# Optimization experiments

Measured on AMD Instinct MI355X. Metric: run time of the kernel, lower is better.

Reference implementation:

```python
import jax, jax.numpy as jnp
import numpy as np

EMBED_DIM = 256
NUM_HEADS = 8
QKV_DIM = EMBED_DIM  # qkv_dim_ratio = 1
HEAD_DIM = QKV_DIM // NUM_HEADS  # 32


def setup_inputs() -> dict:
    key = jax.random.key(0)
    ks = jax.random.split(key, 6)
    B, C, H, W = 1, EMBED_DIM, 64, 64
    s = 0.02
    return {
        "x": jax.random.normal(ks[0], (B, C, H, W), dtype=jnp.float32),
        "wq": jax.random.normal(ks[1], (QKV_DIM, C), dtype=jnp.float32) * s,
        "wk": jax.random.normal(ks[2], (QKV_DIM, C), dtype=jnp.float32) * s,
        "wv": jax.random.normal(ks[3], (QKV_DIM, C), dtype=jnp.float32) * s,
        "wo": jax.random.normal(ks[4], (C, QKV_DIM), dtype=jnp.float32) * s,
        "wl": jax.random.normal(ks[5], (C, 1, 3, 3), dtype=jnp.float32) * s,
    }


def _mhsa(x, wq, wk, wv, wo, wl):
    B, C, H, W = x.shape
    N = H * W
    xf = x.reshape(B, C, N)  # 1x1 conv == channel matmul
    def proj(w):
        # [B, qkv, N] -> [B, heads, N, head_dim]
        y = jnp.einsum('oc,bcn->bon', w, xf)
        return y.reshape(B, NUM_HEADS, HEAD_DIM, N).transpose(0, 1, 3, 2)
    q, k, v = proj(wq), proj(wk), proj(wv)
    scale = HEAD_DIM ** -0.5
    attn = jax.nn.softmax(jnp.einsum('bhnd,bhmd->bhnm', q, k) * scale, axis=-1)
    out = jnp.einsum('bhnm,bhmd->bhnd', attn, v)  # [B, h, N, d]
    out = out.transpose(0, 1, 3, 2).reshape(B, QKV_DIM, N)
    attn_out = jnp.einsum('co,bon->bcn', wo, out).reshape(B, C, H, W)
    local_out = jax.lax.conv_general_dilated(
        x, wl, window_strides=(1, 1), padding=((1, 1), (1, 1)),
        dimension_numbers=('NCHW', 'OIHW', 'NCHW'), feature_group_count=C)
    return local_out + attn_out


def reference(x, wq, wk, wv, wo, wl):
    return _mhsa(x, wq, wk, wv, wo, wl)
```

## Files before the change

### kernel.cpp

```cpp
#include <hip/hip_runtime.h>

#define N_TOK 4096
#define C_DIM 256
#define HEADS 8
#define HDIM  32
#define KSPLIT 4
#define QSCALE 0.17677669529663687f
#define L2E    1.4426950408889634f

typedef __attribute__((ext_vector_type(8))) short bf16x8;
typedef __attribute__((ext_vector_type(4))) float f32x4;
typedef __attribute__((ext_vector_type(4))) unsigned int u32x4;
typedef __attribute__((ext_vector_type(8))) unsigned short u16x8;

static __device__ __forceinline__ unsigned short f2bf(float f) {
  union { float f; unsigned int u; } c; c.f = f;
  return (unsigned short)((c.u + 0x8000u) >> 16);
}
static __device__ __forceinline__ float bf2f(unsigned short u) {
  union { unsigned int i; float f; } c; c.i = ((unsigned int)u) << 16;
  return c.f;
}
static __device__ __forceinline__ float fexp2(float x) {
  float r; asm("v_exp_f32 %0, %1" : "=v"(r) : "v"(x)); return r;
}
static __device__ __forceinline__ unsigned int cvt_pk(float lo, float hi) {
  unsigned int r; asm("v_cvt_pk_bf16_f32 %0, %1, %2" : "=v"(r) : "v"(lo), "v"(hi)); return r;
}

__global__ __launch_bounds__(256) void wsplit(
    const float* __restrict__ wq, const float* __restrict__ wk,
    const float* __restrict__ wv, const float* __restrict__ wo,
    unsigned short* __restrict__ Whi, unsigned short* __restrict__ Wlo)
{
  const int i4  = blockIdx.x * 256 + threadIdx.x;
  const int idx = i4 * 4;
  const int r   = idx >> 8;
  const float* src; int off; float scl = 1.f;
  if (r < 256)      { src = wq; off = idx;          scl = QSCALE * L2E; }
  else if (r < 512) { src = wk; off = idx - 65536;  }
  else if (r < 768) { src = wv; off = idx - 131072; }
  else              { src = wo; off = idx - 196608; }
  float4 v = *reinterpret_cast<const float4*>(&src[off]);
  v.x *= scl; v.y *= scl; v.z *= scl; v.w *= scl;
  ushort4 h, l;
  h.x = f2bf(v.x); l.x = f2bf(v.x - bf2f(h.x));
  h.y = f2bf(v.y); l.y = f2bf(v.y - bf2f(h.y));
  h.z = f2bf(v.z); l.z = f2bf(v.z - bf2f(h.z));
  h.w = f2bf(v.w); l.w = f2bf(v.w - bf2f(h.w));
  *reinterpret_cast<ushort4*>(&Whi[idx]) = h;
  *reinterpret_cast<ushort4*>(&Wlo[idx]) = l;
}

__global__ __launch_bounds__(256) void tsplit(
    const float* __restrict__ src,
    unsigned short* __restrict__ dhi, unsigned short* __restrict__ dlo)
{
  __shared__ float T[64][69];
  const int c0 = blockIdx.y * 64, n0 = blockIdx.x * 64;
  const int t = threadIdx.x;
  {
    const int cl = t >> 2, ng = (t & 3) * 16;
    #pragma unroll
    for (int jj = 0; jj < 4; jj++) {
      const float4 v = *reinterpret_cast<const float4*>(&src[(c0 + cl) * N_TOK + n0 + ng + jj * 4]);
      T[cl][ng + jj * 4 + 0] = v.x; T[cl][ng + jj * 4 + 1] = v.y;
      T[cl][ng + jj * 4 + 2] = v.z; T[cl][ng + jj * 4 + 3] = v.w;
    }
  }
  __syncthreads();
  {
    const int nl = t >> 2, cg = (t & 3) * 16;
    u16x8 h0, h1, l0, l1;
    #pragma unroll
    for (int j = 0; j < 8; j++) {
      const float v = T[cg + j][nl];
      h0[j] = f2bf(v); l0[j] = f2bf(v - bf2f(h0[j]));
    }
    #pragma unroll
    for (int j = 0; j < 8; j++) {
      const float v = T[cg + 8 + j][nl];
      h1[j] = f2bf(v); l1[j] = f2bf(v - bf2f(h1[j]));
    }
    const size_t base = (size_t)(n0 + nl) * C_DIM + c0 + cg;
    *reinterpret_cast<u16x8*>(&dhi[base])     = h0;
    *reinterpret_cast<u16x8*>(&dhi[base + 8]) = h1;
    *reinterpret_cast<u16x8*>(&dlo[base])     = l0;
    *reinterpret_cast<u16x8*>(&dlo[base + 8]) = l1;
  }
}

__global__ __launch_bounds__(256) void qkv_mfma(
    const unsigned short* __restrict__ Whi, const unsigned short* __restrict__ Wlo,
    const unsigned short* __restrict__ Xhi, const unsigned short* __restrict__ Xlo,
    unsigned short* __restrict__ Qkv, unsigned short* __restrict__ Kt)
{
  const int n0 = blockIdx.x * 64;
  const int by = blockIdx.y;
  const int tid = threadIdx.x;
  const int w = tid >> 6, lane = tid & 63, lq = lane & 15, g = lane >> 4;
  const int o0 = by * 64 + w * 16;

  __shared__ unsigned short Bs[2][4096];

  const int e0l = tid & 63, e0f = tid >> 6;
  const unsigned short* s0p; const unsigned short* s1p;
  {
    const int lq_ = e0l & 15, g_ = e0l >> 4;
    const int f0 = e0f, f1 = e0f + 4;
    s0p = ((f0 & 1) ? Xlo : Xhi) + (size_t)(n0 + (f0 >> 1) * 16 + lq_) * C_DIM + 8 * g_;
    s1p = ((f1 & 1) ? Xlo : Xhi) + (size_t)(n0 + (f1 >> 1) * 16 + lq_) * C_DIM + 8 * g_;
  }
  const unsigned short* ahp = &Whi[(size_t)(o0 + lq) * C_DIM + 8 * g];
  const unsigned short* alp = &Wlo[(size_t)(o0 + lq) * C_DIM + 8 * g];

  f32x4 acc[4] = {{0.f,0.f,0.f,0.f},{0.f,0.f,0.f,0.f},{0.f,0.f,0.f,0.f},{0.f,0.f,0.f,0.f}};

  bf16x8 ah = *reinterpret_cast<const bf16x8*>(ahp);
  bf16x8 al = *reinterpret_cast<const bf16x8*>(alp);
  {
    const bf16x8 b0 = *reinterpret_cast<const bf16x8*>(s0p);
    const bf16x8 b1 = *reinterpret_cast<const bf16x8*>(s1p);
    *reinterpret_cast<bf16x8*>(&Bs[0][(size_t)tid * 8]) = b0;
    *reinterpret_cast<bf16x8*>(&Bs[0][((size_t)tid + 256) * 8]) = b1;
  }
  __syncthreads();

  int cur = 0;
  #pragma unroll
  for (int kk = 0; kk < 8; kk++) {
    bf16x8 nb0 = {}, nb1 = {}, nah = {}, nal = {};
    if (kk < 7) {
      const int ko = (kk + 1) * 32;
      nb0 = *reinterpret_cast<const bf16x8*>(s0p + ko);
      nb1 = *reinterpret_cast<const bf16x8*>(s1p + ko);
      nah = *reinterpret_cast<const bf16x8*>(ahp + ko);
      nal = *reinterpret_cast<const bf16x8*>(alp + ko);
    }
    #pragma unroll
    for (int ns = 0; ns < 4; ns++) {
      const bf16x8 bh = *reinterpret_cast<const bf16x8*>(&Bs[cur][(size_t)((ns * 2 + 0) * 64 + lane) * 8]);
      const bf16x8 bl = *reinterpret_cast<const bf16x8*>(&Bs[cur][(size_t)((ns * 2 + 1) * 64 + lane) * 8]);
      acc[ns] = __builtin_amdgcn_mfma_f32_16x16x32_bf16(ah, bh, acc[ns], 0, 0, 0);
      acc[ns] = __builtin_amdgcn_mfma_f32_16x16x32_bf16(ah, bl, acc[ns], 0, 0, 0);
      acc[ns] = __builtin_amdgcn_mfma_f32_16x16x32_bf16(al, bh, acc[ns], 0, 0, 0);
    }
    if (kk < 7) {
      *reinterpret_cast<bf16x8*>(&Bs[cur ^ 1][(size_t)tid * 8]) = nb0;
      *reinterpret_cast<bf16x8*>(&Bs[cur ^ 1][((size_t)tid + 256) * 8]) = nb1;
      ah = nah; al = nal;
    }
    __syncthreads();
    cur ^= 1;
  }

  if (by < 4 || by >= 8) {
    const int orow0 = (by < 4 ? by * 64 : (by - 8) * 64 + 512) + w * 16 + 4 * g;
    #pragma unroll
    for (int ns = 0; ns < 4; ns++)
      #pragma unroll
      for (int r = 0; r < 4; r++)
        Qkv[(size_t)(orow0 + r) * N_TOK + n0 + ns * 16 + lq] = f2bf(acc[ns][r]);
  } else {
    const int ok0 = (by - 4) * 64 + w * 16 + 4 * g;
    const int hh = ok0 >> 5, d0 = ok0 & 31;
    #pragma unroll
    for (int ns = 0; ns < 4; ns++) {
      ushort4 u;
      u.x = f2bf(acc[ns][0]); u.y = f2bf(acc[ns][1]);
      u.z = f2bf(acc[ns][2]); u.w = f2bf(acc[ns][3]);
      *reinterpret_cast<ushort4*>(&Kt[((size_t)hh * N_TOK + n0 + ns * 16 + lq) * HDIM + d0]) = u;
    }
  }
}

__global__ __launch_bounds__(256) void dwconv_kernel(
    const float* __restrict__ x, const float* __restrict__ wl,
    float* __restrict__ out)
{
  const int idx = blockIdx.x * 256 + threadIdx.x;
  const int c  = idx >> 12;
  const int yy = (idx >> 6) & 63;
  const int xx = idx & 63;
  const float* xc = x + c * 4096;
  const float* wc = wl + c * 9;
  float acc = 0.f;
  #pragma unroll
  for (int dy = 0; dy < 3; dy++) {
    const int y = yy + dy - 1;
    if (y < 0 || y > 63) continue;
    #pragma unroll
    for (int dx = 0; dx < 3; dx++) {
      const int x2 = xx + dx - 1;
      if (x2 < 0 || x2 > 63) continue;
      acc += wc[dy * 3 + dx] * xc[y * 64 + x2];
    }
  }
  out[idx] = acc;
}

__global__ __launch_bounds__(256) void attn_mfma(
    const unsigned short* __restrict__ Qkv,
    const unsigned short* __restrict__ Kt,
    float* __restrict__ Opart,
    float* __restrict__ lpart)
{
  const int h  = blockIdx.z;
  const int ks = blockIdx.y;
  const int tid  = threadIdx.x;
  const int w    = tid >> 6;
  const int lane = tid & 63;
  const int lq   = lane & 15;
  const int g    = lane >> 4;
  const int nqa  = blockIdx.x * 128 + w * 32 + lq;
  const int nqb  = nqa + 16;

  __shared__ unsigned short KbL[2][2048];
  __shared__ unsigned short VbL[2][2048];

  bf16x8 qfa, qfb;
  {
    const unsigned short* Qh = Qkv + h * HDIM * N_TOK;
    #pragma unroll
    for (int j = 0; j < 8; j++) {
      qfa[j] = (short)Qh[(8 * g + j) * N_TOK + nqa];
      qfb[j] = (short)Qh[(8 * g + j) * N_TOK + nqb];
    }
  }

  const unsigned short* KtH = Kt + (size_t)h * N_TOK * HDIM;
  const unsigned short* VH  = Qkv + (512 + h * HDIM) * N_TOK;
  const int kbase = ks * (N_TOK / KSPLIT);
  const int pr = 8 * (lq >> 2) + (lq & 3);

  const int skey  = (w & 1) * 4 + (w >> 1) * 32 + pr;
  const unsigned short* ksrc = &KtH[(size_t)(kbase + skey) * HDIM + 8 * g];
  const int sdrow = (w & 1) * 16 + lq;
  const unsigned short* vsrc = &VH[(size_t)sdrow * N_TOK + kbase + (w >> 1) * 32 + 8 * g];

  {
    const bf16x8 kr = *reinterpret_cast<const bf16x8*>(ksrc);
    const bf16x8 vr = *reinterpret_cast<const bf16x8*>(vsrc);
    *reinterpret_cast<bf16x8*>(&KbL[0][tid * 8]) = kr;
    *reinterpret_cast<bf16x8*>(&VbL[0][tid * 8]) = vr;
  }
  __syncthreads();

  f32x4 o0a = {0.f,0.f,0.f,0.f}, o1a = {0.f,0.f,0.f,0.f};
  f32x4 o0b = {0.f,0.f,0.f,0.f}, o1b = {0.f,0.f,0.f,0.f};
  f32x4 laa = {0.f,0.f,0.f,0.f}, lab = {0.f,0.f,0.f,0.f};
  const f32x4 zz = {0.f,0.f,0.f,0.f};
  constexpr int NT = (N_TOK / KSPLIT) / 64;

  int cur = 0;
  #pragma unroll 2
  for (int t = 0; t < NT; ++t) {
    bf16x8 kr = {}, vr = {};
    if (t + 1 < NT) {
      kr = *reinterpret_cast<const bf16x8*>(ksrc + (size_t)(t + 1) * 64 * HDIM);
      vr = *reinterpret_cast<const bf16x8*>(vsrc + (t + 1) * 64);
    }

    const unsigned short* kb = &KbL[cur][0];
    const unsigned short* vb = &VbL[cur][0];
    const bf16x8 kf0 = *reinterpret_cast<const bf16x8*>(&kb[lane * 8]);
    const bf16x8 kf1 = *reinterpret_cast<const bf16x8*>(&kb[lane * 8 + 512]);
    const bf16x8 kf2 = *reinterpret_cast<const bf16x8*>(&kb[lane * 8 + 1024]);
    const bf16x8 kf3 = *reinterpret_cast<const bf16x8*>(&kb[lane * 8 + 1536]);

    f32x4 s0 = __builtin_amdgcn_mfma_f32_16x16x32_bf16(kf0, qfa, zz, 0, 0, 0);
    f32x4 s1 = __builtin_amdgcn_mfma_f32_16x16x32_bf16(kf1, qfa, zz, 0, 0, 0);
    f32x4 s2 = __builtin_amdgcn_mfma_f32_16x16x32_bf16(kf2, qfa, zz, 0, 0, 0);
    f32x4 s3 = __builtin_amdgcn_mfma_f32_16x16x32_bf16(kf3, qfa, zz, 0, 0, 0);
    #pragma unroll
    for (int r = 0; r < 4; r++) {
      s0[r] = fexp2(s0[r]); s1[r] = fexp2(s1[r]);
      s2[r] = fexp2(s2[r]); s3[r] = fexp2(s3[r]);
    }
    laa += s0; laa += s1; laa += s2; laa += s3;
    const u32x4 pua_a = { cvt_pk(s0[0], s0[1]), cvt_pk(s0[2], s0[3]),
                          cvt_pk(s1[0], s1[1]), cvt_pk(s1[2], s1[3]) };
    const u32x4 pub_a = { cvt_pk(s2[0], s2[1]), cvt_pk(s2[2], s2[3]),
                          cvt_pk(s3[0], s3[1]), cvt_pk(s3[2], s3[3]) };
    const bf16x8 pfa_a = __builtin_bit_cast(bf16x8, pua_a);
    const bf16x8 pfb_a = __builtin_bit_cast(bf16x8, pub_a);

    f32x4 t0 = __builtin_amdgcn_mfma_f32_16x16x32_bf16(kf0, qfb, zz, 0, 0, 0);
    f32x4 t1 = __builtin_amdgcn_mfma_f32_16x16x32_bf16(kf1, qfb, zz, 0, 0, 0);
    f32x4 t2 = __builtin_amdgcn_mfma_f32_16x16x32_bf16(kf2, qfb, zz, 0, 0, 0);
    f32x4 t3 = __builtin_amdgcn_mfma_f32_16x16x32_bf16(kf3, qfb, zz, 0, 0, 0);
    #pragma unroll
    for (int r = 0; r < 4; r++) {
      t0[r] = fexp2(t0[r]); t1[r] = fexp2(t1[r]);
      t2[r] = fexp2(t2[r]); t3[r] = fexp2(t3[r]);
    }
    lab += t0; lab += t1; lab += t2; lab += t3;
    const u32x4 pua_b = { cvt_pk(t0[0], t0[1]), cvt_pk(t0[2], t0[3]),
                          cvt_pk(t1[0], t1[1]), cvt_pk(t1[2], t1[3]) };
    const u32x4 pub_b = { cvt_pk(t2[0], t2[1]), cvt_pk(t2[2], t2[3]),
                          cvt_pk(t3[0], t3[1]), cvt_pk(t3[2], t3[3]) };
    const bf16x8 pfa_b = __builtin_bit_cast(bf16x8, pua_b);
    const bf16x8 pfb_b = __builtin_bit_cast(bf16x8, pub_b);

    const bf16x8 vf0a = *reinterpret_cast<const bf16x8*>(&vb[lane * 8]);
    const bf16x8 vf1a = *reinterpret_cast<const bf16x8*>(&vb[lane * 8 + 512]);
    const bf16x8 vf0b = *reinterpret_cast<const bf16x8*>(&vb[lane * 8 + 1024]);
    const bf16x8 vf1b = *reinterpret_cast<const bf16x8*>(&vb[lane * 8 + 1536]);

    o0a = __builtin_amdgcn_mfma_f32_16x16x32_bf16(vf0a, pfa_a, o0a, 0, 0, 0);
    o0a = __builtin_amdgcn_mfma_f32_16x16x32_bf16(vf0b, pfb_a, o0a, 0, 0, 0);
    o1a = __builtin_amdgcn_mfma_f32_16x16x32_bf16(vf1a, pfa_a, o1a, 0, 0, 0);
    o1a = __builtin_amdgcn_mfma_f32_16x16x32_bf16(vf1b, pfb_a, o1a, 0, 0, 0);
    o0b = __builtin_amdgcn_mfma_f32_16x16x32_bf16(vf0a, pfa_b, o0b, 0, 0, 0);
    o0b = __builtin_amdgcn_mfma_f32_16x16x32_bf16(vf0b, pfb_b, o0b, 0, 0, 0);
    o1b = __builtin_amdgcn_mfma_f32_16x16x32_bf16(vf1a, pfa_b, o1b, 0, 0, 0);
    o1b = __builtin_amdgcn_mfma_f32_16x16x32_bf16(vf1b, pfb_b, o1b, 0, 0, 0);

    if (t + 1 < NT) {
      *reinterpret_cast<bf16x8*>(&KbL[cur ^ 1][tid * 8]) = kr;
      *reinterpret_cast<bf16x8*>(&VbL[cur ^ 1][tid * 8]) = vr;
    }
    __syncthreads();
    cur ^= 1;
  }

  float lsa = (laa[0] + laa[1]) + (laa[2] + laa[3]);
  lsa += __shfl_xor(lsa, 16);
  lsa += __shfl_xor(lsa, 32);
  float lsb = (lab[0] + lab[1]) + (lab[2] + lab[3]);
  lsb += __shfl_xor(lsb, 16);
  lsb += __shfl_xor(lsb, 32);

  const int ob = (ks * HEADS + h) * HDIM;
  #pragma unroll
  for (int r = 0; r < 4; r++) {
    Opart[(size_t)(ob + 4 * g + r) * N_TOK + nqa]      = o0a[r];
    Opart[(size_t)(ob + 16 + 4 * g + r) * N_TOK + nqa] = o1a[r];
    Opart[(size_t)(ob + 4 * g + r) * N_TOK + nqb]      = o0b[r];
    Opart[(size_t)(ob + 16 + 4 * g + r) * N_TOK + nqb] = o1b[r];
  }
  if (g == 0) {
    lpart[(ks * HEADS + h) * N_TOK + nqa] = lsa;
    lpart[(ks * HEADS + h) * N_TOK + nqb] = lsb;
  }
}

__global__ __launch_bounds__(256) void combsplit(
    const float* __restrict__ Opart, const float* __restrict__ lpart,
    unsigned short* __restrict__ dhi, unsigned short* __restrict__ dlo)
{
  __shared__ float T[64][69];
  __shared__ float Linv[2][64];
  const int o0 = blockIdx.y * 64, n0 = blockIdx.x * 64;
  const int t = threadIdx.x;
  if (t < 128) {
    const int hl = t >> 6, nl = t & 63;
    const int hh = (o0 >> 5) + hl;
    float L = 0.f;
    #pragma unroll
    for (int ks = 0; ks < KSPLIT; ks++)
      L += lpart[(ks * HEADS + hh) * N_TOK + n0 + nl];
    Linv[hl][nl] = 1.f / L;
  }
  __syncthreads();
  {
    const int cl = t >> 2, ng = (t & 3) * 16;
    const int hrow = cl >> 5;
    #pragma unroll
    for (int jj = 0; jj < 4; jj++) {
      float4 a = make_float4(0.f, 0.f, 0.f, 0.f);
      #pragma unroll
      for (int ks = 0; ks < KSPLIT; ks++) {
        const float4 v = *reinterpret_cast<const float4*>(
            &Opart[(size_t)ks * C_DIM * N_TOK + (size_t)(o0 + cl) * N_TOK + n0 + ng + jj * 4]);
        a.x += v.x; a.y += v.y; a.z += v.z; a.w += v.w;
      }
      T[cl][ng + jj * 4 + 0] = a.x * Linv[hrow][ng + jj * 4 + 0];
      T[cl][ng + jj * 4 + 1] = a.y * Linv[hrow][ng + jj * 4 + 1];
      T[cl][ng + jj * 4 + 2] = a.z * Linv[hrow][ng + jj * 4 + 2];
      T[cl][ng + jj * 4 + 3] = a.w * Linv[hrow][ng + jj * 4 + 3];
    }
  }
  __syncthreads();
  {
    const int nl = t >> 2, cg = (t & 3) * 16;
    u16x8 h0, h1, l0, l1;
    #pragma unroll
    for (int j = 0; j < 8; j++) {
      const float v = T[cg + j][nl];
      h0[j] = f2bf(v); l0[j] = f2bf(v - bf2f(h0[j]));
    }
    #pragma unroll
    for (int j = 0; j < 8; j++) {
      const float v = T[cg + 8 + j][nl];
      h1[j] = f2bf(v); l1[j] = f2bf(v - bf2f(h1[j]));
    }
    const size_t base = (size_t)(n0 + nl) * C_DIM + o0 + cg;
    *reinterpret_cast<u16x8*>(&dhi[base])     = h0;
    *reinterpret_cast<u16x8*>(&dhi[base + 8]) = h1;
    *reinterpret_cast<u16x8*>(&dlo[base])     = l0;
    *reinterpret_cast<u16x8*>(&dlo[base + 8]) = l1;
  }
}

__global__ __launch_bounds__(256) void out_mfma(
    const unsigned short* __restrict__ Whi, const unsigned short* __restrict__ Wlo,
    const unsigned short* __restrict__ Ohi, const unsigned short* __restrict__ Olo,
    float* __restrict__ out)
{
  const int n0 = blockIdx.x * 64;
  const int by = blockIdx.y;
  const int kb = blockIdx.z * 128;
  const int tid = threadIdx.x;
  const int w = tid >> 6, lane = tid & 63, lq = lane & 15, g = lane >> 4;
  const int c0 = by * 64 + w * 16;

  __shared__ unsigned short Bs[2][4096];

  const int e0l = tid & 63, e0f = tid >> 6;
  const unsigned short* s0p; const unsigned short* s1p;
  {
    const int lq_ = e0l & 15, g_ = e0l >> 4;
    const int f0 = e0f, f1 = e0f + 4;
    s0p = ((f0 & 1) ? Olo : Ohi) + (size_t)(n0 + (f0 >> 1) * 16 + lq_) * C_DIM + kb + 8 * g_;
    s1p = ((f1 & 1) ? Olo : Ohi) + (size_t)(n0 + (f1 >> 1) * 16 + lq_) * C_DIM + kb + 8 * g_;
  }
  const unsigned short* ahp = &Whi[(size_t)(768 + c0 + lq) * C_DIM + kb + 8 * g];
  const unsigned short* alp = &Wlo[(size_t)(768 + c0 + lq) * C_DIM + kb + 8 * g];

  f32x4 acc[4] = {{0.f,0.f,0.f,0.f},{0.f,0.f,0.f,0.f},{0.f,0.f,0.f,0.f},{0.f,0.f,0.f,0.f}};

  bf16x8 ah = *reinterpret_cast<const bf16x8*>(ahp);
  bf16x8 al = *reinterpret_cast<const bf16x8*>(alp);
  {
    const bf16x8 b0 = *reinterpret_cast<const bf16x8*>(s0p);
    const bf16x8 b1 = *reinterpret_cast<const bf16x8*>(s1p);
    *reinterpret_cast<bf16x8*>(&Bs[0][(size_t)tid * 8]) = b0;
    *reinterpret_cast<bf16x8*>(&Bs[0][((size_t)tid + 256) * 8]) = b1;
  }
  __syncthreads();

  int cur = 0;
  #pragma unroll
  for (int kk = 0; kk < 4; kk++) {
    bf16x8 nb0 = {}, nb1 = {}, nah = {}, nal = {};
    if (kk < 3) {
      const int ko = (kk + 1) * 32;
      nb0 = *reinterpret_cast<const bf16x8*>(s0p + ko);
      nb1 = *reinterpret_cast<const bf16x8*>(s1p + ko);
      nah = *reinterpret_cast<const bf16x8*>(ahp + ko);
      nal = *reinterpret_cast<const bf16x8*>(alp + ko);
    }
    #pragma unroll
    for (int ns = 0; ns < 4; ns++) {
      const bf16x8 bh = *reinterpret_cast<const bf16x8*>(&Bs[cur][(size_t)((ns * 2 + 0) * 64 + lane) * 8]);
      const bf16x8 bl = *reinterpret_cast<const bf16x8*>(&Bs[cur][(size_t)((ns * 2 + 1) * 64 + lane) * 8]);
      acc[ns] = __builtin_amdgcn_mfma_f32_16x16x32_bf16(ah, bh, acc[ns], 0, 0, 0);
      acc[ns] = __builtin_amdgcn_mfma_f32_16x16x32_bf16(ah, bl, acc[ns], 0, 0, 0);
      acc[ns] = __builtin_amdgcn_mfma_f32_16x16x32_bf16(al, bh, acc[ns], 0, 0, 0);
    }
    if (kk < 3) {
      *reinterpret_cast<bf16x8*>(&Bs[cur ^ 1][(size_t)tid * 8]) = nb0;
      *reinterpret_cast<bf16x8*>(&Bs[cur ^ 1][((size_t)tid + 256) * 8]) = nb1;
      ah = nah; al = nal;
    }
    __syncthreads();
    cur ^= 1;
  }

  #pragma unroll
  for (int ns = 0; ns < 4; ns++)
    #pragma unroll
    for (int r = 0; r < 4; r++)
      unsafeAtomicAdd(&out[(size_t)(c0 + 4 * g + r) * N_TOK + n0 + ns * 16 + lq], acc[ns][r]);
}

extern "C" void kernel_launch(void* const* d_in, const int* in_sizes, int n_in,
                              void* d_out, int out_size, void* d_ws, size_t ws_size,
                              hipStream_t stream) {
  const float* x  = (const float*)d_in[0];
  const float* wq = (const float*)d_in[1];
  const float* wk = (const float*)d_in[2];
  const float* wv = (const float*)d_in[3];
  const float* wo = (const float*)d_in[4];
  const float* wl = (const float*)d_in[5];
  float* out = (float*)d_out;

  float* Opart = (float*)d_ws;
  float* lpart = Opart + (size_t)KSPLIT * C_DIM * N_TOK;
  unsigned short* Qkv = (unsigned short*)(lpart + KSPLIT * HEADS * N_TOK);
  unsigned short* Kt  = Qkv + 768 * N_TOK;
  unsigned short* Whi = Kt + (size_t)HEADS * N_TOK * HDIM;
  unsigned short* Wlo = Whi + 1024 * C_DIM;
  unsigned short* Xhi = Wlo + 1024 * C_DIM;
  unsigned short* Xlo = Xhi + (size_t)N_TOK * C_DIM;
  unsigned short* Ohi = Xlo + (size_t)N_TOK * C_DIM;
  unsigned short* Olo = Ohi + (size_t)N_TOK * C_DIM;

  wsplit<<<256, 256, 0, stream>>>(wq, wk, wv, wo, Whi, Wlo);
  tsplit<<<dim3(64, 4), 256, 0, stream>>>(x, Xhi, Xlo);
  qkv_mfma<<<dim3(64, 12), 256, 0, stream>>>(Whi, Wlo, Xhi, Xlo, Qkv, Kt);
  dwconv_kernel<<<4096, 256, 0, stream>>>(x, wl, out);
  attn_mfma<<<dim3(32, KSPLIT, HEADS), 256, 0, stream>>>(Qkv, Kt, Opart, lpart);
  combsplit<<<dim3(64, 4), 256, 0, stream>>>(Opart, lpart, Ohi, Olo);
  out_mfma<<<dim3(64, 4, 2), 256, 0, stream>>>(Whi, Wlo, Ohi, Olo, out);
}
```

Before: 142.5 us.

## Drop split-bf16 precision, fuse prep and dwconv, double attention KSPLIT

Removes the hi/lo bf16 splitting of weights, inputs and attention output, so the QKV and output projections run 2 MFMAs per k-step instead of 3 and move half the bytes. The weight and input prep kernels are merged into one launch. The depthwise conv is folded into the out_mfma epilogue, which now writes directly instead of using atomics and a K-split. Attention partials are stored as bf16 and KSPLIT goes from 4 to 8 for more parallelism. The cost is lower numerical accuracy, plus more partial sums to combine.

```diff
diff --git a/kernel.cpp b/kernel.cpp
--- a/kernel.cpp
+++ b/kernel.cpp
@@ -4,7 +4,7 @@
 #define C_DIM 256
 #define HEADS 8
 #define HDIM  32
-#define KSPLIT 4
+#define KSPLIT 8
 #define QSCALE 0.17677669529663687f
 #define L2E    1.4426950408889634f
 
@@ -28,71 +28,58 @@
   unsigned int r; asm("v_cvt_pk_bf16_f32 %0, %1, %2" : "=v"(r) : "v"(lo), "v"(hi)); return r;
 }
 
-__global__ __launch_bounds__(256) void wsplit(
+__global__ __launch_bounds__(256) void prep(
     const float* __restrict__ wq, const float* __restrict__ wk,
     const float* __restrict__ wv, const float* __restrict__ wo,
-    unsigned short* __restrict__ Whi, unsigned short* __restrict__ Wlo)
-{
-  const int i4  = blockIdx.x * 256 + threadIdx.x;
-  const int idx = i4 * 4;
-  const int r   = idx >> 8;
-  const float* src; int off; float scl = 1.f;
-  if (r < 256)      { src = wq; off = idx;          scl = QSCALE * L2E; }
-  else if (r < 512) { src = wk; off = idx - 65536;  }
-  else if (r < 768) { src = wv; off = idx - 131072; }
-  else              { src = wo; off = idx - 196608; }
-  float4 v = *reinterpret_cast<const float4*>(&src[off]);
-  v.x *= scl; v.y *= scl; v.z *= scl; v.w *= scl;
-  ushort4 h, l;
-  h.x = f2bf(v.x); l.x = f2bf(v.x - bf2f(h.x));
-  h.y = f2bf(v.y); l.y = f2bf(v.y - bf2f(h.y));
-  h.z = f2bf(v.z); l.z = f2bf(v.z - bf2f(h.z));
-  h.w = f2bf(v.w); l.w = f2bf(v.w - bf2f(h.w));
-  *reinterpret_cast<ushort4*>(&Whi[idx]) = h;
-  *reinterpret_cast<ushort4*>(&Wlo[idx]) = l;
-}
-
-__global__ __launch_bounds__(256) void tsplit(
-    const float* __restrict__ src,
-    unsigned short* __restrict__ dhi, unsigned short* __restrict__ dlo)
+    const float* __restrict__ x,
+    unsigned short* __restrict__ Wb, unsigned short* __restrict__ Xb)
 {
   __shared__ float T[64][69];
-  const int c0 = blockIdx.y * 64, n0 = blockIdx.x * 64;
+  const int bid = blockIdx.x;
   const int t = threadIdx.x;
-  {
-    const int cl = t >> 2, ng = (t & 3) * 16;
-    #pragma unroll
-    for (int jj = 0; jj < 4; jj++) {
-      const float4 v = *reinterpret_cast<const float4*>(&src[(c0 + cl) * N_TOK + n0 + ng + jj * 4]);
-      T[cl][ng + jj * 4 + 0] = v.x; T[cl][ng + jj * 4 + 1] = v.y;
-      T[cl][ng + jj * 4 + 2] = v.z; T[cl][ng + jj * 4 + 3] = v.w;
-    }
-  }
-  __syncthreads();
-  {
-    const int nl = t >> 2, cg = (t & 3) * 16;
-    u16x8 h0, h1, l0, l1;
-    #pragma unroll
-    for (int j = 0; j < 8; j++) {
-      const float v = T[cg + j][nl];
-      h0[j] = f2bf(v); l0[j] = f2bf(v - bf2f(h0[j]));
-    }
-    #pragma unroll
-    for (int j = 0; j < 8; j++) {
-      const float v = T[cg + 8 + j][nl];
-      h1[j] = f2bf(v); l1[j] = f2bf(v - bf2f(h1[j]));
-    }
-    const size_t base = (size_t)(n0 + nl) * C_DIM + c0 + cg;
-    *reinterpret_cast<u16x8*>(&dhi[base])     = h0;
-    *reinterpret_cast<u16x8*>(&dhi[base + 8]) = h1;
-    *reinterpret_cast<u16x8*>(&dlo[base])     = l0;
-    *reinterpret_cast<u16x8*>(&dlo[base + 8]) = l1;
+  if (bid < 256) {
+    const int idx = (bid * 256 + t) * 4;
+    const int r   = idx >> 8;
+    const float* src; int off; float scl = 1.f;
+    if (r < 256)      { src = wq; off = idx;          scl = QSCALE * L2E; }
+    else if (r < 512) { src = wk; off = idx - 65536;  }
+    else if (r < 768) { src = wv; off = idx - 131072; }
+    else              { src = wo; off = idx - 196608; }
+    float4 v = *reinterpret_cast<const float4*>(&src[off]);
+    ushort4 h;
+    h.x = f2bf(v.x * scl); h.y = f2bf(v.y * scl);
+    h.z = f2bf(v.z * scl); h.w = f2bf(v.w * scl);
+    *reinterpret_cast<ushort4*>(&Wb[idx]) = h;
+  } else {
+    const int b2 = bid - 256;
+    const int n0 = (b2 & 63) * 64, c0 = (b2 >> 6) * 64;
+    {
+      const int cl = t >> 2, ng = (t & 3) * 16;
+      #pragma unroll
+      for (int jj = 0; jj < 4; jj++) {
+        const float4 v = *reinterpret_cast<const float4*>(&x[(c0 + cl) * N_TOK + n0 + ng + jj * 4]);
+        T[cl][ng + jj * 4 + 0] = v.x; T[cl][ng + jj * 4 + 1] = v.y;
+        T[cl][ng + jj * 4 + 2] = v.z; T[cl][ng + jj * 4 + 3] = v.w;
+      }
+    }
+    __syncthreads();
+    {
+      const int nl = t >> 2, cg = (t & 3) * 16;
+      u16x8 h0, h1;
+      #pragma unroll
+      for (int j = 0; j < 8; j++) h0[j] = f2bf(T[cg + j][nl]);
+      #pragma unroll
+      for (int j = 0; j < 8; j++) h1[j] = f2bf(T[cg + 8 + j][nl]);
+      const size_t base = (size_t)(n0 + nl) * C_DIM + c0 + cg;
+      *reinterpret_cast<u16x8*>(&Xb[base])     = h0;
+      *reinterpret_cast<u16x8*>(&Xb[base + 8]) = h1;
+    }
   }
 }
 
 __global__ __launch_bounds__(256) void qkv_mfma(
-    const unsigned short* __restrict__ Whi, const unsigned short* __restrict__ Wlo,
-    const unsigned short* __restrict__ Xhi, const unsigned short* __restrict__ Xlo,
+    const unsigned short* __restrict__ Wb,
+    const unsigned short* __restrict__ Xb,
     unsigned short* __restrict__ Qkv, unsigned short* __restrict__ Kt)
 {
   const int n0 = blockIdx.x * 64;
@@ -103,24 +90,17 @@
 
   __shared__ unsigned short Bs[2][4096];
 
-  const int e0l = tid & 63, e0f = tid >> 6;
-  const unsigned short* s0p; const unsigned short* s1p;
-  {
-    const int lq_ = e0l & 15, g_ = e0l >> 4;
-    const int f0 = e0f, f1 = e0f + 4;
-    s0p = ((f0 & 1) ? Xlo : Xhi) + (size_t)(n0 + (f0 >> 1) * 16 + lq_) * C_DIM + 8 * g_;
-    s1p = ((f1 & 1) ? Xlo : Xhi) + (size_t)(n0 + (f1 >> 1) * 16 + lq_) * C_DIM + 8 * g_;
-  }
-  const unsigned short* ahp = &Whi[(size_t)(o0 + lq) * C_DIM + 8 * g];
-  const unsigned short* alp = &Wlo[(size_t)(o0 + lq) * C_DIM + 8 * g];
+  const int lane_ = tid & 63, ns_ = tid >> 6;
+  const unsigned short* sp = Xb + (size_t)(n0 + ns_ * 16 + (lane_ & 15)) * C_DIM + 8 * (lane_ >> 4);
+  const unsigned short* ahp = &Wb[(size_t)(o0 + lq) * C_DIM + 8 * g];
 
   f32x4 acc[4] = {{0.f,0.f,0.f,0.f},{0.f,0.f,0.f,0.f},{0.f,0.f,0.f,0.f},{0.f,0.f,0.f,0.f}};
 
-  bf16x8 ah = *reinterpret_cast<const bf16x8*>(ahp);
-  bf16x8 al = *reinterpret_cast<const bf16x8*>(alp);
-  {
-    const bf16x8 b0 = *reinterpret_cast<const bf16x8*>(s0p);
-    const bf16x8 b1 = *reinterpret_cast<const bf16x8*>(s1p);
+  bf16x8 ah0 = *reinterpret_cast<const bf16x8*>(ahp);
+  bf16x8 ah1 = *reinterpret_cast<const bf16x8*>(ahp + 32);
+  {
+    const bf16x8 b0 = *reinterpret_cast<const bf16x8*>(sp);
+    const bf16x8 b1 = *reinterpret_cast<const bf16x8*>(sp + 32);
     *reinterpret_cast<bf16x8*>(&Bs[0][(size_t)tid * 8]) = b0;
     *reinterpret_cast<bf16x8*>(&Bs[0][((size_t)tid + 256) * 8]) = b1;
   }
@@ -128,27 +108,26 @@
 
   int cur = 0;
   #pragma unroll
-  for (int kk = 0; kk < 8; kk++) {
-    bf16x8 nb0 = {}, nb1 = {}, nah = {}, nal = {};
-    if (kk < 7) {
-      const int ko = (kk + 1) * 32;
-      nb0 = *reinterpret_cast<const bf16x8*>(s0p + ko);
-      nb1 = *reinterpret_cast<const bf16x8*>(s1p + ko);
-      nah = *reinterpret_cast<const bf16x8*>(ahp + ko);
-      nal = *reinterpret_cast<const bf16x8*>(alp + ko);
+  for (int kk = 0; kk < 4; kk++) {
+    bf16x8 nb0 = {}, nb1 = {}, nah0 = {}, nah1 = {};
+    if (kk < 3) {
+      const int ko = (kk + 1) * 64;
+      nb0  = *reinterpret_cast<const bf16x8*>(sp + ko);
+      nb1  = *reinterpret_cast<const bf16x8*>(sp + ko + 32);
+      nah0 = *reinterpret_cast<const bf16x8*>(ahp + ko);
+      nah1 = *reinterpret_cast<const bf16x8*>(ahp + ko + 32);
     }
     #pragma unroll
     for (int ns = 0; ns < 4; ns++) {
-      const bf16x8 bh = *reinterpret_cast<const bf16x8*>(&Bs[cur][(size_t)((ns * 2 + 0) * 64 + lane) * 8]);
-      const bf16x8 bl = *reinterpret_cast<const bf16x8*>(&Bs[cur][(size_t)((ns * 2 + 1) * 64 + lane) * 8]);
-      acc[ns] = __builtin_amdgcn_mfma_f32_16x16x32_bf16(ah, bh, acc[ns], 0, 0, 0);
-      acc[ns] = __builtin_amdgcn_mfma_f32_16x16x32_bf16(ah, bl, acc[ns], 0, 0, 0);
-      acc[ns] = __builtin_amdgcn_mfma_f32_16x16x32_bf16(al, bh, acc[ns], 0, 0, 0);
-    }
-    if (kk < 7) {
+      const bf16x8 bh0 = *reinterpret_cast<const bf16x8*>(&Bs[cur][(size_t)(ns * 64 + lane) * 8]);
+      const bf16x8 bh1 = *reinterpret_cast<const bf16x8*>(&Bs[cur][(size_t)((ns + 4) * 64 + lane) * 8]);
+      acc[ns] = __builtin_amdgcn_mfma_f32_16x16x32_bf16(ah0, bh0, acc[ns], 0, 0, 0);
+      acc[ns] = __builtin_amdgcn_mfma_f32_16x16x32_bf16(ah1, bh1, acc[ns], 0, 0, 0);
+    }
+    if (kk < 3) {
       *reinterpret_cast<bf16x8*>(&Bs[cur ^ 1][(size_t)tid * 8]) = nb0;
       *reinterpret_cast<bf16x8*>(&Bs[cur ^ 1][((size_t)tid + 256) * 8]) = nb1;
-      ah = nah; al = nal;
+      ah0 = nah0; ah1 = nah1;
     }
     __syncthreads();
     cur ^= 1;
@@ -174,35 +153,10 @@
   }
 }
 
-__global__ __launch_bounds__(256) void dwconv_kernel(
-    const float* __restrict__ x, const float* __restrict__ wl,
-    float* __restrict__ out)
-{
-  const int idx = blockIdx.x * 256 + threadIdx.x;
-  const int c  = idx >> 12;
-  const int yy = (idx >> 6) & 63;
-  const int xx = idx & 63;
-  const float* xc = x + c * 4096;
-  const float* wc = wl + c * 9;
-  float acc = 0.f;
-  #pragma unroll
-  for (int dy = 0; dy < 3; dy++) {
-    const int y = yy + dy - 1;
-    if (y < 0 || y > 63) continue;
-    #pragma unroll
-    for (int dx = 0; dx < 3; dx++) {
-      const int x2 = xx + dx - 1;
-      if (x2 < 0 || x2 > 63) continue;
-      acc += wc[dy * 3 + dx] * xc[y * 64 + x2];
-    }
-  }
-  out[idx] = acc;
-}
-
 __global__ __launch_bounds__(256) void attn_mfma(
     const unsigned short* __restrict__ Qkv,
     const unsigned short* __restrict__ Kt,
-    float* __restrict__ Opart,
+    unsigned short* __restrict__ Opb,
     float* __restrict__ lpart)
 {
   const int h  = blockIdx.z;
@@ -334,10 +288,10 @@
   const int ob = (ks * HEADS + h) * HDIM;
   #pragma unroll
   for (int r = 0; r < 4; r++) {
-    Opart[(size_t)(ob + 4 * g + r) * N_TOK + nqa]      = o0a[r];
-    Opart[(size_t)(ob + 16 + 4 * g + r) * N_TOK + nqa] = o1a[r];
-    Opart[(size_t)(ob + 4 * g + r) * N_TOK + nqb]      = o0b[r];
-    Opart[(size_t)(ob + 16 + 4 * g + r) * N_TOK + nqb] = o1b[r];
+    Opb[(size_t)(ob + 4 * g + r) * N_TOK + nqa]      = f2bf(o0a[r]);
+    Opb[(size_t)(ob + 16 + 4 * g + r) * N_TOK + nqa] = f2bf(o1a[r]);
+    Opb[(size_t)(ob + 4 * g + r) * N_TOK + nqb]      = f2bf(o0b[r]);
+    Opb[(size_t)(ob + 16 + 4 * g + r) * N_TOK + nqb] = f2bf(o1b[r]);
   }
   if (g == 0) {
     lpart[(ks * HEADS + h) * N_TOK + nqa] = lsa;
@@ -346,8 +300,8 @@
 }
 
 __global__ __launch_bounds__(256) void combsplit(
-    const float* __restrict__ Opart, const float* __restrict__ lpart,
-    unsigned short* __restrict__ dhi, unsigned short* __restrict__ dlo)
+    const unsigned short* __restrict__ Opb, const float* __restrict__ lpart,
+    unsigned short* __restrict__ Ob)
 {
   __shared__ float T[64][69];
   __shared__ float Linv[2][64];
@@ -368,73 +322,58 @@
     const int hrow = cl >> 5;
     #pragma unroll
     for (int jj = 0; jj < 4; jj++) {
-      float4 a = make_float4(0.f, 0.f, 0.f, 0.f);
+      float a0 = 0.f, a1 = 0.f, a2 = 0.f, a3 = 0.f;
       #pragma unroll
       for (int ks = 0; ks < KSPLIT; ks++) {
-        const float4 v = *reinterpret_cast<const float4*>(
-            &Opart[(size_t)ks * C_DIM * N_TOK + (size_t)(o0 + cl) * N_TOK + n0 + ng + jj * 4]);
-        a.x += v.x; a.y += v.y; a.z += v.z; a.w += v.w;
+        const ushort4 u = *reinterpret_cast<const ushort4*>(
+            &Opb[(size_t)ks * C_DIM * N_TOK + (size_t)(o0 + cl) * N_TOK + n0 + ng + jj * 4]);
+        a0 += bf2f(u.x); a1 += bf2f(u.y); a2 += bf2f(u.z); a3 += bf2f(u.w);
       }
-      T[cl][ng + jj * 4 + 0] = a.x * Linv[hrow][ng + jj * 4 + 0];
-      T[cl][ng + jj * 4 + 1] = a.y * Linv[hrow][ng + jj * 4 + 1];
-      T[cl][ng + jj * 4 + 2] = a.z * Linv[hrow][ng + jj * 4 + 2];
-      T[cl][ng + jj * 4 + 3] = a.w * Linv[hrow][ng + jj * 4 + 3];
+      T[cl][ng + jj * 4 + 0] = a0 * Linv[hrow][ng + jj * 4 + 0];
+      T[cl][ng + jj * 4 + 1] = a1 * Linv[hrow][ng + jj * 4 + 1];
+      T[cl][ng + jj * 4 + 2] = a2 * Linv[hrow][ng + jj * 4 + 2];
+      T[cl][ng + jj * 4 + 3] = a3 * Linv[hrow][ng + jj * 4 + 3];
     }
   }
   __syncthreads();
   {
     const int nl = t >> 2, cg = (t & 3) * 16;
-    u16x8 h0, h1, l0, l1;
-    #pragma unroll
-    for (int j = 0; j < 8; j++) {
-      const float v = T[cg + j][nl];
-      h0[j] = f2bf(v); l0[j] = f2bf(v - bf2f(h0[j]));
-    }
-    #pragma unroll
-    for (int j = 0; j < 8; j++) {
-      const float v = T[cg + 8 + j][nl];
-      h1[j] = f2bf(v); l1[j] = f2bf(v - bf2f(h1[j]));
-    }
+    u16x8 h0, h1;
+    #pragma unroll
+    for (int j = 0; j < 8; j++) h0[j] = f2bf(T[cg + j][nl]);
+    #pragma unroll
+    for (int j = 0; j < 8; j++) h1[j] = f2bf(T[cg + 8 + j][nl]);
     const size_t base = (size_t)(n0 + nl) * C_DIM + o0 + cg;
-    *reinterpret_cast<u16x8*>(&dhi[base])     = h0;
-    *reinterpret_cast<u16x8*>(&dhi[base + 8]) = h1;
-    *reinterpret_cast<u16x8*>(&dlo[base])     = l0;
-    *reinterpret_cast<u16x8*>(&dlo[base + 8]) = l1;
+    *reinterpret_cast<u16x8*>(&Ob[base])     = h0;
+    *reinterpret_cast<u16x8*>(&Ob[base + 8]) = h1;
   }
 }
 
 __global__ __launch_bounds__(256) void out_mfma(
-    const unsigned short* __restrict__ Whi, const unsigned short* __restrict__ Wlo,
-    const unsigned short* __restrict__ Ohi, const unsigned short* __restrict__ Olo,
+    const unsigned short* __restrict__ Wb,
+    const unsigned short* __restrict__ Ob,
+    const float* __restrict__ x, const float* __restrict__ wl,
     float* __restrict__ out)
 {
   const int n0 = blockIdx.x * 64;
   const int by = blockIdx.y;
-  const int kb = blockIdx.z * 128;
   const int tid = threadIdx.x;
   const int w = tid >> 6, lane = tid & 63, lq = lane & 15, g = lane >> 4;
   const int c0 = by * 64 + w * 16;
 
   __shared__ unsigned short Bs[2][4096];
 
-  const int e0l = tid & 63, e0f = tid >> 6;
-  const unsigned short* s0p; const unsigned short* s1p;
-  {
-    const int lq_ = e0l & 15, g_ = e0l >> 4;
-    const int f0 = e0f, f1 = e0f + 4;
-    s0p = ((f0 & 1) ? Olo : Ohi) + (size_t)(n0 + (f0 >> 1) * 16 + lq_) * C_DIM + kb + 8 * g_;
-    s1p = ((f1 & 1) ? Olo : Ohi) + (size_t)(n0 + (f1 >> 1) * 16 + lq_) * C_DIM + kb + 8 * g_;
-  }
-  const unsigned short* ahp = &Whi[(size_t)(768 + c0 + lq) * C_DIM + kb + 8 * g];
-  const unsigned short* alp = &Wlo[(size_t)(768 + c0 + lq) * C_DIM + kb + 8 * g];
+  const int lane_ = tid & 63, ns_ = tid >> 6;
+  const unsigned short* sp = Ob + (size_t)(n0 + ns_ * 16 + (lane_ & 15)) * C_DIM + 8 * (lane_ >> 4);
+  const unsigned short* ahp = &Wb[(size_t)(768 + c0 + lq) * C_DIM + 8 * g];
 
   f32x4 acc[4] = {{0.f,0.f,0.f,0.f},{0.f,0.f,0.f,0.f},{0.f,0.f,0.f,0.f},{0.f,0.f,0.f,0.f}};
 
-  bf16x8 ah = *reinterpret_cast<const bf16x8*>(ahp);
-  bf16x8 al = *reinterpret_cast<const bf16x8*>(alp);
-  {
-    const bf16x8 b0 = *reinterpret_cast<const bf16x8*>(s0p);
-    const bf16x8 b1 = *reinterpret_cast<const bf16x8*>(s1p);
+  bf16x8 ah0 = *reinterpret_cast<const bf16x8*>(ahp);
+  bf16x8 ah1 = *reinterpret_cast<const bf16x8*>(ahp + 32);
+  {
+    const bf16x8 b0 = *reinterpret_cast<const bf16x8*>(sp);
+    const bf16x8 b1 = *reinterpret_cast<const bf16x8*>(sp + 32);
     *reinterpret_cast<bf16x8*>(&Bs[0][(size_t)tid * 8]) = b0;
     *reinterpret_cast<bf16x8*>(&Bs[0][((size_t)tid + 256) * 8]) = b1;
   }
@@ -443,36 +382,55 @@
   int cur = 0;
   #pragma unroll
   for (int kk = 0; kk < 4; kk++) {
-    bf16x8 nb0 = {}, nb1 = {}, nah = {}, nal = {};
+    bf16x8 nb0 = {}, nb1 = {}, nah0 = {}, nah1 = {};
     if (kk < 3) {
-      const int ko = (kk + 1) * 32;
-      nb0 = *reinterpret_cast<const bf16x8*>(s0p + ko);
-      nb1 = *reinterpret_cast<const bf16x8*>(s1p + ko);
-      nah = *reinterpret_cast<const bf16x8*>(ahp + ko);
-      nal = *reinterpret_cast<const bf16x8*>(alp + ko);
+      const int ko = (kk + 1) * 64;
+      nb0  = *reinterpret_cast<const bf16x8*>(sp + ko);
+      nb1  = *reinterpret_cast<const bf16x8*>(sp + ko + 32);
+      nah0 = *reinterpret_cast<const bf16x8*>(ahp + ko);
+      nah1 = *reinterpret_cast<const bf16x8*>(ahp + ko + 32);
     }
     #pragma unroll
     for (int ns = 0; ns < 4; ns++) {
-      const bf16x8 bh = *reinterpret_cast<const bf16x8*>(&Bs[cur][(size_t)((ns * 2 + 0) * 64 + lane) * 8]);
-      const bf16x8 bl = *reinterpret_cast<const bf16x8*>(&Bs[cur][(size_t)((ns * 2 + 1) * 64 + lane) * 8]);
-      acc[ns] = __builtin_amdgcn_mfma_f32_16x16x32_bf16(ah, bh, acc[ns], 0, 0, 0);
-      acc[ns] = __builtin_amdgcn_mfma_f32_16x16x32_bf16(ah, bl, acc[ns], 0, 0, 0);
-      acc[ns] = __builtin_amdgcn_mfma_f32_16x16x32_bf16(al, bh, acc[ns], 0, 0, 0);
+      const bf16x8 bh0 = *reinterpret_cast<const bf16x8*>(&Bs[cur][(size_t)(ns * 64 + lane) * 8]);
+      const bf16x8 bh1 = *reinterpret_cast<const bf16x8*>(&Bs[cur][(size_t)((ns + 4) * 64 + lane) * 8]);
+      acc[ns] = __builtin_amdgcn_mfma_f32_16x16x32_bf16(ah0, bh0, acc[ns], 0, 0, 0);
+      acc[ns] = __builtin_amdgcn_mfma_f32_16x16x32_bf16(ah1, bh1, acc[ns], 0, 0, 0);
     }
     if (kk < 3) {
       *reinterpret_cast<bf16x8*>(&Bs[cur ^ 1][(size_t)tid * 8]) = nb0;
       *reinterpret_cast<bf16x8*>(&Bs[cur ^ 1][((size_t)tid + 256) * 8]) = nb1;
-      ah = nah; al = nal;
+      ah0 = nah0; ah1 = nah1;
     }
     __syncthreads();
     cur ^= 1;
   }
 
+  const int yy = blockIdx.x;
   #pragma unroll
-  for (int ns = 0; ns < 4; ns++)
-    #pragma unroll
-    for (int r = 0; r < 4; r++)
-      unsafeAtomicAdd(&out[(size_t)(c0 + 4 * g + r) * N_TOK + n0 + ns * 16 + lq], acc[ns][r]);
+  for (int ns = 0; ns < 4; ns++) {
+    #pragma unroll
+    for (int r = 0; r < 4; r++) {
+      const int c = c0 + 4 * g + r;
+      const int n = n0 + ns * 16 + lq;
+      const int xx = n & 63;
+      const float* xc  = x + (size_t)c * 4096;
+      const float* wl9 = wl + (size_t)c * 9;
+      float cv = 0.f;
+      #pragma unroll
+      for (int dy = 0; dy < 3; dy++) {
+        const int y2 = yy + dy - 1;
+        if (y2 < 0 || y2 > 63) continue;
+        #pragma unroll
+        for (int dx = 0; dx < 3; dx++) {
+          const int x2 = xx + dx - 1;
+          if (x2 < 0 || x2 > 63) continue;
+          cv += wl9[dy * 3 + dx] * xc[y2 * 64 + x2];
+        }
+      }
+      out[(size_t)c * N_TOK + n] = cv + acc[ns][r];
+    }
+  }
 }
 
 extern "C" void kernel_launch(void* const* d_in, const int* in_sizes, int n_in,
@@ -486,22 +444,17 @@
   const float* wl = (const float*)d_in[5];
   float* out = (float*)d_out;
 
-  float* Opart = (float*)d_ws;
-  float* lpart = Opart + (size_t)KSPLIT * C_DIM * N_TOK;
+  unsigned short* Opb = (unsigned short*)d_ws;
+  float* lpart = (float*)(Opb + (size_t)KSPLIT * C_DIM * N_TOK);
   unsigned short* Qkv = (unsigned short*)(lpart + KSPLIT * HEADS * N_TOK);
   unsigned short* Kt  = Qkv + 768 * N_TOK;
-  unsigned short* Whi = Kt + (size_t)HEADS * N_TOK * HDIM;
-  unsigned short* Wlo = Whi + 1024 * C_DIM;
-  unsigned short* Xhi = Wlo + 1024 * C_DIM;
-  unsigned short* Xlo = Xhi + (size_t)N_TOK * C_DIM;
-  unsigned short* Ohi = Xlo + (size_t)N_TOK * C_DIM;
-  unsigned short* Olo = Ohi + (size_t)N_TOK * C_DIM;
-
-  wsplit<<<256, 256, 0, stream>>>(wq, wk, wv, wo, Whi, Wlo);
-  tsplit<<<dim3(64, 4), 256, 0, stream>>>(x, Xhi, Xlo);
-  qkv_mfma<<<dim3(64, 12), 256, 0, stream>>>(Whi, Wlo, Xhi, Xlo, Qkv, Kt);
-  dwconv_kernel<<<4096, 256, 0, stream>>>(x, wl, out);
-  attn_mfma<<<dim3(32, KSPLIT, HEADS), 256, 0, stream>>>(Qkv, Kt, Opart, lpart);
-  combsplit<<<dim3(64, 4), 256, 0, stream>>>(Opart, lpart, Ohi, Olo);
-  out_mfma<<<dim3(64, 4, 2), 256, 0, stream>>>(Whi, Wlo, Ohi, Olo, out);
-}
+  unsigned short* Wb  = Kt + (size_t)HEADS * N_TOK * HDIM;
+  unsigned short* Xb  = Wb + 1024 * C_DIM;
+  unsigned short* Ob  = Xb + (size_t)N_TOK * C_DIM;
+
+  prep<<<512, 256, 0, stream>>>(wq, wk, wv, wo, x, Wb, Xb);
+  qkv_mfma<<<dim3(64, 12), 256, 0, stream>>>(Wb, Xb, Qkv, Kt);
+  attn_mfma<<<dim3(32, KSPLIT, HEADS), 256, 0, stream>>>(Qkv, Kt, Opb, lpart);
+  combsplit<<<dim3(64, 4), 256, 0, stream>>>(Opb, lpart, Ob);
+  out_mfma<<<dim3(64, 4), 256, 0, stream>>>(Wb, Ob, x, wl, out);
+}
```

Result: faster. 131.9 us (-7.5%).
